# Kernel tuning notes

Hardware: AMD Instinct MI355X
Metric: run time of the kernel (lower is better)

## Reference

```python
import jax, jax.numpy as jnp
import numpy as np

# ---- module constants (from init_kwargs) ----
VOXEL_SIZE = np.array([0.1, 0.1, 0.2], np.float32)
PC_RANGE = np.array([0.0, -40.0, -3.0, 70.4, 40.0, 1.0], np.float32)
MAX_PTS = 10            # max_points_in_voxel
MAX_VOX = 40000         # max_voxel_num (hard voxelization cap per sample)
GRID = np.round((PC_RANGE[3:] - PC_RANGE[:3]) / VOXEL_SIZE).astype(np.int32)  # [704,800,20] (x,y,z)
BIG = int(GRID[0]) * int(GRID[1]) * int(GRID[2])

PC_MIN = jnp.asarray(PC_RANGE[:3])
VSIZE = jnp.asarray(VOXEL_SIZE)
GRID_J = jnp.asarray(GRID)

B = 8
N_PER_B = 120000


def setup_inputs() -> dict:
    key = jax.random.key(0)
    k1, = jax.random.split(key, 1)
    u = jax.random.uniform(k1, (B * N_PER_B, 4), dtype=jnp.float32)
    # place points inside (and slightly around) pc_range
    x = u[:, 0] * 72.0 - 0.5
    y = u[:, 1] * 82.0 - 41.0
    z = u[:, 2] * 4.4 - 3.2
    inten = u[:, 3]
    bs_idx = jnp.repeat(jnp.arange(B, dtype=jnp.float32), N_PER_B)
    points = jnp.stack([bs_idx, x, y, z, inten], axis=1)  # [960000, 5]
    return {"points": points, "batch_size": B}


def _voxelize_one(pts):
    """Hard voxelization of one point cloud pts [N,4] -> fixed-size buffers.
    Faithful to first-come voxel ordering and per-voxel point caps."""
    N = pts.shape[0]
    idxs = jnp.arange(N, dtype=jnp.int32)
    xyz = pts[:, :3]
    c = jnp.floor((xyz - PC_MIN) / VSIZE).astype(jnp.int32)  # [N,3] (x,y,z)
    valid = jnp.all((c >= 0) & (c < GRID_J), axis=1)
    lid = (c[:, 2] * GRID[1] + c[:, 1]) * GRID[0] + c[:, 0]  # z-major linear id
    lid = jnp.where(valid, lid, BIG)

    order = jnp.argsort(lid)            # stable: within a voxel, original order kept
    lid_s = lid[order]
    is_new = jnp.concatenate([jnp.ones((1,), bool), lid_s[1:] != lid_s[:-1]])
    gid = jnp.cumsum(is_new.astype(jnp.int32)) - 1           # group id per sorted point
    starts = jax.lax.cummax(jnp.where(is_new, idxs, 0))      # group start position
    pos = idxs - starts                                      # rank inside its voxel

    g_lid = jax.ops.segment_min(lid_s, gid, num_segments=N)
    g_valid = g_lid < BIG
    first_orig = jax.ops.segment_min(order.astype(jnp.int32), gid, num_segments=N)
    # voxel slot = first-appearance rank (invalid/empty groups pushed to the end)
    first_key = jnp.where(g_valid, first_orig, N + idxs)
    perm = jnp.argsort(first_key)
    slot = jnp.zeros(N, jnp.int32).at[perm].set(idxs)

    pslot = slot[gid]
    keep = g_valid[gid] & (pslot < MAX_VOX) & (pos < MAX_PTS)
    sslot = jnp.where(keep, pslot, MAX_VOX)   # overflow bucket, sliced off
    spos = jnp.where(keep, pos, 0)
    voxels = jnp.zeros((MAX_VOX + 1, MAX_PTS, pts.shape[1]), pts.dtype)
    voxels = voxels.at[sslot, spos].set(pts[order])[:MAX_VOX]

    gcount = jax.ops.segment_sum(keep.astype(jnp.int32), gid, num_segments=N)
    gslot = jnp.where(g_valid & (slot < MAX_VOX), slot, MAX_VOX)
    num_points = jnp.zeros(MAX_VOX + 1, jnp.int32).at[gslot].set(gcount)[:MAX_VOX]

    cs = c[order]
    gz = jax.ops.segment_min(cs[:, 2], gid, num_segments=N)
    gy = jax.ops.segment_min(cs[:, 1], gid, num_segments=N)
    gx = jax.ops.segment_min(cs[:, 0], gid, num_segments=N)
    coors = jnp.full((MAX_VOX + 1, 3), -1, jnp.int32)
    coors = coors.at[gslot].set(jnp.stack([gz, gy, gx], axis=1))[:MAX_VOX]  # (z,y,x)
    return voxels, num_points, coors


def reference(points, batch_size):
    feats = points[:, 1:]
    n_per_b = feats.shape[0] // batch_size  # points constructed contiguously per sample
    pts = feats.reshape(batch_size, n_per_b, feats.shape[1])
    voxels_b, num_b, coors_b = jax.vmap(_voxelize_one)(pts)
    voxels = voxels_b.reshape(batch_size * MAX_VOX, MAX_PTS, feats.shape[1])
    num_points = num_b.reshape(-1)
    batch_col = jnp.repeat(jnp.arange(batch_size, dtype=jnp.int32), MAX_VOX)[:, None]
    coors_batch = jnp.concatenate([batch_col, coors_b.reshape(-1, 3)], axis=1)  # [b,z,y,x]
    grid_size = jnp.asarray(GRID)
    return voxels, num_points, coors_batch, grid_size
```

## Files before the change

kernel.cpp:

```cpp
#include <hip/hip_runtime.h>

#define NB        8
#define NPB       120000
#define NPTS      (NB * NPB)
#define MAX_PTS   10
#define MAX_VOX   40000
#define GX        704
#define GY        800
#define GZ        20
#define CELLS     (GX * GY * GZ)
#define WPB       (CELLS / 32)

#define HC2       (1 << 15)
#define HMASK2    (HC2 - 1)
#define NSLOT2    (NB * HC2)
#define TILES     469
#define TILES_PAD 512
#define MBCAP     8192
#define MTILE     2048

#define EMPTY64   0xFFFFFFFFFFFFFFFFull

#define OUT_VOX   0LL
#define OUT_NUM   12800000LL
#define OUT_COOR  13120000LL
#define OUT_GRID  14400000LL

__device__ __forceinline__ bool point_cell(const float* __restrict__ p,
                                           int& cx, int& cy, int& cz) {
    cx = (int)floorf((p[1] - 0.0f)   / 0.1f);
    cy = (int)floorf((p[2] - (-40.0f)) / 0.1f);
    cz = (int)floorf((p[3] - (-3.0f))  / 0.2f);
    return (cx >= 0) & (cx < GX) & (cy >= 0) & (cy < GY) & (cz >= 0) & (cz < GZ);
}

__global__ void k_init(float* __restrict__ out, uint4* __restrict__ bm4,
                       ulonglong2* __restrict__ slab2, unsigned* __restrict__ mcount) {
    int t = blockIdx.x * blockDim.x + threadIdx.x;
    int stride = gridDim.x * blockDim.x;
    uint4 z4 = make_uint4(0u, 0u, 0u, 0u);
    for (int i = t; i < NB * WPB / 4; i += stride) bm4[i] = z4;
    ulonglong2 e2; e2.x = EMPTY64; e2.y = EMPTY64;
    for (int i = t; i < NSLOT2 / 2; i += stride) slab2[i] = e2;
    if (t < NB) mcount[t * 16] = 0u;
    if (t == 0) {
        out[OUT_GRID + 0] = 704.f;
        out[OUT_GRID + 1] = 800.f;
        out[OUT_GRID + 2] = 20.f;
    }
}

__global__ void k_phase1(const float* __restrict__ pts, unsigned* __restrict__ bm,
                         unsigned long long* __restrict__ slabB,
                         unsigned char* __restrict__ flag, int* __restrict__ lid32) {
    int b = blockIdx.x & 7;
    int idx = (blockIdx.x >> 3) * 256 + threadIdx.x;
    if (idx >= NPB) return;
    int g = b * NPB + idx;
    const float* p = pts + (long long)g * 5;
    int cx, cy, cz;
    if (!point_cell(p, cx, cy, cz)) { flag[g] = 0; lid32[g] = -1; return; }
    int lid = (cz * GY + cy) * GX + cx;
    lid32[g] = lid;
    unsigned mask = 1u << (lid & 31);
    unsigned old = atomicOr(&bm[b * WPB + (lid >> 5)], mask);
    if ((old & mask) == 0u) {
        flag[g] = 1;
    } else {
        flag[g] = 0;
        unsigned h = (((unsigned)lid * 2654435761u) >> 17) & HMASK2;
        unsigned long long key = ((unsigned long long)(unsigned)lid << 32)
                               | (unsigned long long)(unsigned)idx;
        int base2 = b * HC2;
        while (true) {
            unsigned long long* wp = &slabB[base2 + (int)h];
            unsigned long long cur = *((volatile unsigned long long*)wp);
            if (cur == EMPTY64) {
                unsigned long long o = atomicCAS(wp, EMPTY64, key);
                if (o == EMPTY64) break;
                cur = o;
            }
            if ((unsigned)(cur >> 32) == (unsigned)lid) { atomicMin(wp, key); break; }
            h = (h + 1) & HMASK2;
        }
    }
}

__global__ void k_phase2(const int* __restrict__ lid32, unsigned char* __restrict__ flag,
                         unsigned long long* __restrict__ slabB) {
    int b = blockIdx.x & 7;
    int idx = (blockIdx.x >> 3) * 256 + threadIdx.x;
    if (idx >= NPB) return;
    int g = b * NPB + idx;
    if (!flag[g]) return;
    int lid = lid32[g];
    unsigned h = (((unsigned)lid * 2654435761u) >> 17) & HMASK2;
    int base2 = b * HC2;
    while (true) {
        unsigned long long cur = slabB[base2 + (int)h];
        if (cur == EMPTY64) break;
        if ((unsigned)(cur >> 32) == (unsigned)lid) {
            unsigned long long key = ((unsigned long long)(unsigned)lid << 32)
                                   | (unsigned long long)(unsigned)idx;
            unsigned long long old = atomicMin(&slabB[base2 + (int)h], key);
            unsigned omin = (unsigned)old;
            if (omin < (unsigned)idx) {
                flag[g] = 0;
                flag[b * NPB + (int)omin] = 2;
            } else {
                flag[g] = 2;
            }
            break;
        }
        h = (h + 1) & HMASK2;
    }
}

__global__ void k_leader_scan(const unsigned char* __restrict__ flag,
                              unsigned char* __restrict__ rank8, int* __restrict__ tileSum) {
    int b = blockIdx.y;
    int tile = blockIdx.x;
    int idx = tile * 256 + threadIdx.x;
    int f = 0;
    if (idx < NPB) f = flag[b * NPB + idx] ? 1 : 0;
    __shared__ int sc[256];
    sc[threadIdx.x] = f;
    __syncthreads();
    for (int off = 1; off < 256; off <<= 1) {
        int v = sc[threadIdx.x];
        if ((int)threadIdx.x >= off) v += sc[threadIdx.x - off];
        __syncthreads();
        sc[threadIdx.x] = v;
        __syncthreads();
    }
    if (idx < NPB) rank8[b * NPB + idx] = (unsigned char)(sc[threadIdx.x] - f);
    if (threadIdx.x == 255) tileSum[b * TILES_PAD + tile] = sc[255];
}

__global__ void k_scan_tiles(const int* __restrict__ tileSum, int* __restrict__ tileOff) {
    int b = blockIdx.x;
    int t = threadIdx.x;
    __shared__ int sc[512];
    int v = (t < TILES) ? tileSum[b * TILES_PAD + t] : 0;
    sc[t] = v;
    __syncthreads();
    for (int off = 1; off < 512; off <<= 1) {
        int x = sc[t];
        if (t >= off) x += sc[t - off];
        __syncthreads();
        sc[t] = x;
        __syncthreads();
    }
    if (t < TILES) tileOff[b * TILES_PAD + t] = sc[t] - v;
}

__global__ void k_finish(const float* __restrict__ pts, const unsigned char* __restrict__ flag,
                         const int* __restrict__ lid32,
                         const unsigned char* __restrict__ rank8, const int* __restrict__ tileOff,
                         const unsigned long long* __restrict__ slabB,
                         float* __restrict__ out, int2* __restrict__ mlist,
                         unsigned* __restrict__ mcount) {
    int b = blockIdx.x & 7;
    int idx = (blockIdx.x >> 3) * 256 + threadIdx.x;
    if (idx >= NPB) return;
    int g = b * NPB + idx;
    int lid = lid32[g];
    if (lid < 0) return;
    unsigned char fl = flag[g];
    if (fl) {
        int slot = tileOff[b * TILES_PAD + (idx >> 8)] + (int)rank8[g];
        if (slot >= MAX_VOX) return;
        unsigned ul = (unsigned)lid;
        unsigned cx = ul % (unsigned)GX;
        unsigned tt = ul / (unsigned)GX;
        unsigned cy = tt % (unsigned)GY;
        unsigned cz = tt / (unsigned)GY;
        long long r = (long long)b * MAX_VOX + slot;
        ((float4*)(out + OUT_COOR))[r] = make_float4((float)b, (float)cz, (float)cy, (float)cx);
        out[OUT_NUM + r] = 1.f;
        const float* p = pts + (long long)g * 5;
        float4* row = (float4*)(out + OUT_VOX + r * (MAX_PTS * 4));
        row[0] = make_float4(p[1], p[2], p[3], p[4]);
        float4 zf = make_float4(0.f, 0.f, 0.f, 0.f);
        #pragma unroll
        for (int i = 1; i < MAX_PTS; i++) row[i] = zf;
    } else {
        unsigned h = (((unsigned)lid * 2654435761u) >> 17) & HMASK2;
        int base2 = b * HC2;
        unsigned minidx;
        while (true) {
            unsigned long long cur = slabB[base2 + (int)h];
            if ((unsigned)(cur >> 32) == (unsigned)lid) { minidx = (unsigned)cur; break; }
            h = (h + 1) & HMASK2;
        }
        int slot = tileOff[b * TILES_PAD + ((int)minidx >> 8)] + (int)rank8[b * NPB + (int)minidx];
        if (slot >= MAX_VOX) return;
        unsigned m = atomicAdd(&mcount[b * 16], 1u);
        if (m < MBCAP) mlist[(size_t)b * MBCAP + m] = make_int2(slot, idx);
    }
}

__global__ void k_multi(const float* __restrict__ pts,
                        const int2* __restrict__ mlist, const unsigned* __restrict__ mcount,
                        float* __restrict__ out) {
    int b = blockIdx.y;
    unsigned n = mcount[b * 16];
    if (n > MBCAP) n = MBCAP;
    unsigned t = blockIdx.x * blockDim.x + threadIdx.x;
    const int2* lst = mlist + (size_t)b * MBCAP;
    bool active = (t < n);
    int2 e = active ? lst[t] : make_int2(-1, -1);
    int pos = 1;
    int same = 0;
    __shared__ int2 sm[MTILE];
    for (unsigned chunk = 0; chunk < n; chunk += MTILE) {
        unsigned m = n - chunk;
        if (m > MTILE) m = MTILE;
        for (unsigned i = threadIdx.x; i < m; i += 256)
            sm[i] = lst[chunk + i];
        __syncthreads();
        if (active) {
            #pragma unroll 4
            for (unsigned j = 0; j < m; j++) {
                int2 o = sm[j];
                if (o.x == e.x) { same++; if (o.y < e.y) pos++; }
            }
        }
        __syncthreads();
    }
    if (!active) return;
    if (pos == 1) {
        int cnt = same + 1;
        out[OUT_NUM + (long long)b * MAX_VOX + e.x] =
            (float)(cnt < MAX_PTS ? cnt : MAX_PTS);
    }
    if (pos >= MAX_PTS) return;
    const float* p = pts + ((long long)b * NPB + e.y) * 5;
    ((float4*)(out + OUT_VOX))[(long long)(b * MAX_VOX + e.x) * MAX_PTS + pos] =
        make_float4(p[1], p[2], p[3], p[4]);
}

extern "C" void kernel_launch(void* const* d_in, const int* in_sizes, int n_in,
                              void* d_out, int out_size, void* d_ws, size_t ws_size,
                              hipStream_t stream) {
    const float* pts = (const float*)d_in[0];
    float* out = (float*)d_out;

    char* w = (char*)d_ws;
    unsigned* bm = (unsigned*)w;              w += (size_t)NB * WPB * 4;
    unsigned long long* slabB = (unsigned long long*)w;
    w += (size_t)NSLOT2 * 8;
    unsigned char* flag = (unsigned char*)w;  w += (size_t)NPTS;
    unsigned char* rank8 = (unsigned char*)w; w += (size_t)NPTS;
    int* lid32 = (int*)w;    w += (size_t)NPTS * 4;
    int* tileSum = (int*)w;  w += (size_t)NB * TILES_PAD * 4;
    int* tileOff = (int*)w;  w += (size_t)NB * TILES_PAD * 4;
    int2* mlist = (int2*)w;  w += (size_t)NB * MBCAP * 8;
    unsigned* mcount = (unsigned*)w; w += (size_t)NB * 16 * 4;

    const int PB = TILES * NB;
    k_init<<<dim3(2048), dim3(256), 0, stream>>>(out, (uint4*)bm, (ulonglong2*)slabB, mcount);
    k_phase1<<<dim3(PB), dim3(256), 0, stream>>>(pts, bm, slabB, flag, lid32);
    k_phase2<<<dim3(PB), dim3(256), 0, stream>>>(lid32, flag, slabB);
    k_leader_scan<<<dim3(TILES, NB), dim3(256), 0, stream>>>(flag, rank8, tileSum);
    k_scan_tiles<<<dim3(NB), dim3(512), 0, stream>>>(tileSum, tileOff);
    k_finish<<<dim3(PB), dim3(256), 0, stream>>>(pts, flag, lid32, rank8, tileOff, slabB, out, mlist, mcount);
    k_multi<<<dim3(MBCAP / 256, NB), dim3(256), 0, stream>>>(pts, mlist, mcount, out);
}
```

Measured before the change: 161.7 us.

## Replace bitmap+two-phase leader detection with single hash-table insert and fused scans

Removes the per-sample occupancy bitmap (about 8 x 11.26M bits, which had to be zeroed every call) and instead inserts every valid point into a larger per-sample open-addressing hash table keyed by voxel id, using atomicMin to keep the first point index. Leader detection moves into the rank-scan kernel through a hash lookup, and the tile-offset scan is folded into k_finish, with each block redoing the small scan. This drops the bitmap clear, the flag array and two kernel launches. In exchange it adds more hash traffic and atomics on a larger table (2M slots, 16 MB to initialise) plus repeated probing in later kernels.

```diff
diff --git a/kernel.cpp b/kernel.cpp
--- a/kernel.cpp
+++ b/kernel.cpp
@@ -9,11 +9,11 @@
 #define GY        800
 #define GZ        20
 #define CELLS     (GX * GY * GZ)
-#define WPB       (CELLS / 32)
-
-#define HC2       (1 << 15)
+
+#define HC2       (1 << 18)
 #define HMASK2    (HC2 - 1)
 #define NSLOT2    (NB * HC2)
+
 #define TILES     469
 #define TILES_PAD 512
 #define MBCAP     8192
@@ -34,12 +34,14 @@
     return (cx >= 0) & (cx < GX) & (cy >= 0) & (cy < GY) & (cz >= 0) & (cz < GZ);
 }
 
-__global__ void k_init(float* __restrict__ out, uint4* __restrict__ bm4,
-                       ulonglong2* __restrict__ slab2, unsigned* __restrict__ mcount) {
+__device__ __forceinline__ unsigned cell_hash(int lid) {
+    return (((unsigned)lid * 2654435761u) >> 14) & HMASK2;
+}
+
+__global__ void k_init(float* __restrict__ out, ulonglong2* __restrict__ slab2,
+                       unsigned* __restrict__ mcount) {
     int t = blockIdx.x * blockDim.x + threadIdx.x;
     int stride = gridDim.x * blockDim.x;
-    uint4 z4 = make_uint4(0u, 0u, 0u, 0u);
-    for (int i = t; i < NB * WPB / 4; i += stride) bm4[i] = z4;
     ulonglong2 e2; e2.x = EMPTY64; e2.y = EMPTY64;
     for (int i = t; i < NSLOT2 / 2; i += stride) slab2[i] = e2;
     if (t < NB) mcount[t * 16] = 0u;
@@ -50,79 +52,58 @@
     }
 }
 
-__global__ void k_phase1(const float* __restrict__ pts, unsigned* __restrict__ bm,
+__global__ void k_insert(const float* __restrict__ pts,
                          unsigned long long* __restrict__ slabB,
-                         unsigned char* __restrict__ flag, int* __restrict__ lid32) {
+                         int* __restrict__ lid32) {
     int b = blockIdx.x & 7;
     int idx = (blockIdx.x >> 3) * 256 + threadIdx.x;
     if (idx >= NPB) return;
     int g = b * NPB + idx;
     const float* p = pts + (long long)g * 5;
     int cx, cy, cz;
-    if (!point_cell(p, cx, cy, cz)) { flag[g] = 0; lid32[g] = -1; return; }
+    if (!point_cell(p, cx, cy, cz)) { lid32[g] = -1; return; }
     int lid = (cz * GY + cy) * GX + cx;
     lid32[g] = lid;
-    unsigned mask = 1u << (lid & 31);
-    unsigned old = atomicOr(&bm[b * WPB + (lid >> 5)], mask);
-    if ((old & mask) == 0u) {
-        flag[g] = 1;
-    } else {
-        flag[g] = 0;
-        unsigned h = (((unsigned)lid * 2654435761u) >> 17) & HMASK2;
-        unsigned long long key = ((unsigned long long)(unsigned)lid << 32)
-                               | (unsigned long long)(unsigned)idx;
-        int base2 = b * HC2;
-        while (true) {
-            unsigned long long* wp = &slabB[base2 + (int)h];
-            unsigned long long cur = *((volatile unsigned long long*)wp);
-            if (cur == EMPTY64) {
-                unsigned long long o = atomicCAS(wp, EMPTY64, key);
-                if (o == EMPTY64) break;
-                cur = o;
-            }
-            if ((unsigned)(cur >> 32) == (unsigned)lid) { atomicMin(wp, key); break; }
-            h = (h + 1) & HMASK2;
-        }
-    }
-}
-
-__global__ void k_phase2(const int* __restrict__ lid32, unsigned char* __restrict__ flag,
-                         unsigned long long* __restrict__ slabB) {
+    unsigned h = cell_hash(lid);
+    unsigned long long key = ((unsigned long long)(unsigned)lid << 32)
+                           | (unsigned long long)(unsigned)idx;
+    unsigned long long* base = slabB + (size_t)b * HC2;
+    while (true) {
+        unsigned long long cur = *((volatile unsigned long long*)(base + h));
+        if (cur == EMPTY64) {
+            unsigned long long o = atomicCAS(base + h, EMPTY64, key);
+            if (o == EMPTY64) break;
+            cur = o;
+        }
+        if ((unsigned)(cur >> 32) == (unsigned)lid) {
+            if ((unsigned)cur > (unsigned)idx) atomicMin(base + h, key);
+            break;
+        }
+        h = (h + 1) & HMASK2;
+    }
+}
+
+__global__ void k_rankscan(const int* __restrict__ lid32,
+                           const unsigned long long* __restrict__ slabB,
+                           unsigned char* __restrict__ rank8, int* __restrict__ tileSum) {
     int b = blockIdx.x & 7;
-    int idx = (blockIdx.x >> 3) * 256 + threadIdx.x;
-    if (idx >= NPB) return;
-    int g = b * NPB + idx;
-    if (!flag[g]) return;
-    int lid = lid32[g];
-    unsigned h = (((unsigned)lid * 2654435761u) >> 17) & HMASK2;
-    int base2 = b * HC2;
-    while (true) {
-        unsigned long long cur = slabB[base2 + (int)h];
-        if (cur == EMPTY64) break;
-        if ((unsigned)(cur >> 32) == (unsigned)lid) {
-            unsigned long long key = ((unsigned long long)(unsigned)lid << 32)
-                                   | (unsigned long long)(unsigned)idx;
-            unsigned long long old = atomicMin(&slabB[base2 + (int)h], key);
-            unsigned omin = (unsigned)old;
-            if (omin < (unsigned)idx) {
-                flag[g] = 0;
-                flag[b * NPB + (int)omin] = 2;
-            } else {
-                flag[g] = 2;
-            }
-            break;
-        }
-        h = (h + 1) & HMASK2;
-    }
-}
-
-__global__ void k_leader_scan(const unsigned char* __restrict__ flag,
-                              unsigned char* __restrict__ rank8, int* __restrict__ tileSum) {
-    int b = blockIdx.y;
-    int tile = blockIdx.x;
+    int tile = blockIdx.x >> 3;
     int idx = tile * 256 + threadIdx.x;
     int f = 0;
-    if (idx < NPB) f = flag[b * NPB + idx] ? 1 : 0;
+    if (idx < NPB) {
+        int lid = lid32[b * NPB + idx];
+        if (lid >= 0) {
+            const unsigned long long* base = slabB + (size_t)b * HC2;
+            unsigned h = cell_hash(lid);
+            unsigned long long cur;
+            while (true) {
+                cur = base[h];
+                if ((unsigned)(cur >> 32) == (unsigned)lid) break;
+                h = (h + 1) & HMASK2;
+            }
+            f = ((unsigned)cur == (unsigned)idx) ? 1 : 0;
+        }
+    }
     __shared__ int sc[256];
     sc[threadIdx.x] = f;
     __syncthreads();
@@ -137,38 +118,53 @@
     if (threadIdx.x == 255) tileSum[b * TILES_PAD + tile] = sc[255];
 }
 
-__global__ void k_scan_tiles(const int* __restrict__ tileSum, int* __restrict__ tileOff) {
-    int b = blockIdx.x;
-    int t = threadIdx.x;
-    __shared__ int sc[512];
-    int v = (t < TILES) ? tileSum[b * TILES_PAD + t] : 0;
-    sc[t] = v;
-    __syncthreads();
-    for (int off = 1; off < 512; off <<= 1) {
-        int x = sc[t];
-        if (t >= off) x += sc[t - off];
-        __syncthreads();
-        sc[t] = x;
-        __syncthreads();
-    }
-    if (t < TILES) tileOff[b * TILES_PAD + t] = sc[t] - v;
-}
-
-__global__ void k_finish(const float* __restrict__ pts, const unsigned char* __restrict__ flag,
-                         const int* __restrict__ lid32,
-                         const unsigned char* __restrict__ rank8, const int* __restrict__ tileOff,
+__global__ void k_finish(const float* __restrict__ pts, const int* __restrict__ lid32,
+                         const unsigned char* __restrict__ rank8,
+                         const int* __restrict__ tileSum,
                          const unsigned long long* __restrict__ slabB,
                          float* __restrict__ out, int2* __restrict__ mlist,
                          unsigned* __restrict__ mcount) {
     int b = blockIdx.x & 7;
-    int idx = (blockIdx.x >> 3) * 256 + threadIdx.x;
+    int tile = blockIdx.x >> 3;
+    int t = threadIdx.x;
+
+    __shared__ int sc[256];
+    __shared__ int soff[TILES_PAD];
+    int v0 = (2 * t     < TILES) ? tileSum[b * TILES_PAD + 2 * t]     : 0;
+    int v1 = (2 * t + 1 < TILES) ? tileSum[b * TILES_PAD + 2 * t + 1] : 0;
+    int w = v0 + v1;
+    sc[t] = w;
+    __syncthreads();
+    for (int off = 1; off < 256; off <<= 1) {
+        int x = sc[t];
+        if (t >= off) x += sc[t - off];
+        __syncthreads();
+        sc[t] = x;
+        __syncthreads();
+    }
+    int e = sc[t] - w;
+    soff[2 * t] = e;
+    soff[2 * t + 1] = e + v0;
+    __syncthreads();
+
+    int idx = tile * 256 + t;
     if (idx >= NPB) return;
     int g = b * NPB + idx;
     int lid = lid32[g];
     if (lid < 0) return;
-    unsigned char fl = flag[g];
-    if (fl) {
-        int slot = tileOff[b * TILES_PAD + (idx >> 8)] + (int)rank8[g];
+
+    const unsigned long long* base = slabB + (size_t)b * HC2;
+    unsigned h = cell_hash(lid);
+    unsigned long long cur;
+    while (true) {
+        cur = base[h];
+        if ((unsigned)(cur >> 32) == (unsigned)lid) break;
+        h = (h + 1) & HMASK2;
+    }
+    unsigned minidx = (unsigned)cur;
+
+    if (minidx == (unsigned)idx) {
+        int slot = soff[idx >> 8] + (int)rank8[g];
         if (slot >= MAX_VOX) return;
         unsigned ul = (unsigned)lid;
         unsigned cx = ul % (unsigned)GX;
@@ -185,15 +181,7 @@
         #pragma unroll
         for (int i = 1; i < MAX_PTS; i++) row[i] = zf;
     } else {
-        unsigned h = (((unsigned)lid * 2654435761u) >> 17) & HMASK2;
-        int base2 = b * HC2;
-        unsigned minidx;
-        while (true) {
-            unsigned long long cur = slabB[base2 + (int)h];
-            if ((unsigned)(cur >> 32) == (unsigned)lid) { minidx = (unsigned)cur; break; }
-            h = (h + 1) & HMASK2;
-        }
-        int slot = tileOff[b * TILES_PAD + ((int)minidx >> 8)] + (int)rank8[b * NPB + (int)minidx];
+        int slot = soff[(int)minidx >> 8] + (int)rank8[b * NPB + (int)minidx];
         if (slot >= MAX_VOX) return;
         unsigned m = atomicAdd(&mcount[b * 16], 1u);
         if (m < MBCAP) mlist[(size_t)b * MBCAP + m] = make_int2(slot, idx);
@@ -247,23 +235,18 @@
     float* out = (float*)d_out;
 
     char* w = (char*)d_ws;
-    unsigned* bm = (unsigned*)w;              w += (size_t)NB * WPB * 4;
     unsigned long long* slabB = (unsigned long long*)w;
     w += (size_t)NSLOT2 * 8;
-    unsigned char* flag = (unsigned char*)w;  w += (size_t)NPTS;
     unsigned char* rank8 = (unsigned char*)w; w += (size_t)NPTS;
     int* lid32 = (int*)w;    w += (size_t)NPTS * 4;
     int* tileSum = (int*)w;  w += (size_t)NB * TILES_PAD * 4;
-    int* tileOff = (int*)w;  w += (size_t)NB * TILES_PAD * 4;
     int2* mlist = (int2*)w;  w += (size_t)NB * MBCAP * 8;
     unsigned* mcount = (unsigned*)w; w += (size_t)NB * 16 * 4;
 
     const int PB = TILES * NB;
-    k_init<<<dim3(2048), dim3(256), 0, stream>>>(out, (uint4*)bm, (ulonglong2*)slabB, mcount);
-    k_phase1<<<dim3(PB), dim3(256), 0, stream>>>(pts, bm, slabB, flag, lid32);
-    k_phase2<<<dim3(PB), dim3(256), 0, stream>>>(lid32, flag, slabB);
-    k_leader_scan<<<dim3(TILES, NB), dim3(256), 0, stream>>>(flag, rank8, tileSum);
-    k_scan_tiles<<<dim3(NB), dim3(512), 0, stream>>>(tileSum, tileOff);
-    k_finish<<<dim3(PB), dim3(256), 0, stream>>>(pts, flag, lid32, rank8, tileOff, slabB, out, mlist, mcount);
+    k_init<<<dim3(2048), dim3(256), 0, stream>>>(out, (ulonglong2*)slabB, mcount);
+    k_insert<<<dim3(PB), dim3(256), 0, stream>>>(pts, slabB, lid32);
+    k_rankscan<<<dim3(PB), dim3(256), 0, stream>>>(lid32, slabB, rank8, tileSum);
+    k_finish<<<dim3(PB), dim3(256), 0, stream>>>(pts, lid32, rank8, tileSum, slabB, out, mlist, mcount);
     k_multi<<<dim3(MBCAP / 256, NB), dim3(256), 0, stream>>>(pts, mlist, mcount, out);
 }
```

Result: slower. 185.5 us (+14.7%).
